# Optimization experiments

Measured on AMD Instinct MI355X. Metric: run time of the kernel, lower is better.

The kernel has to match this reference:

```python
import jax, jax.numpy as jnp
import numpy as np

B, S, H, NH = 2, 2048, 1024, 16
HD = H // NH
R = 4
LORA_SCALE = 16.0 / 4.0  # lora_alpha / r


def lora_linear(x, W, b, A, Bm):
    # x: [b,t,in]; W: [out,in]; A: [r,in]; Bm: [out,r]
    base = jnp.einsum('bti,oi->bto', x, W) + b
    lora = jnp.einsum('btr,or->bto', jnp.einsum('bti,ri->btr', x, A), Bm)
    return base + LORA_SCALE * lora


def setup_inputs() -> dict:
    key = jax.random.key(0)
    ks = jax.random.split(key, 14)
    std = 1.0 / np.sqrt(H)
    d = {
        'hidden_states': jax.random.normal(ks[0], (B, S, H), dtype=jnp.float32),
        'attention_mask': jnp.zeros((B, 1, 1, S), dtype=jnp.float32),
    }
    for i, nm in enumerate(['q', 'k', 'v']):
        d[f'W{nm}'] = jax.random.normal(ks[1 + 4 * i], (H, H), dtype=jnp.float32) * std
        d[f'b{nm}'] = jnp.zeros((H,), dtype=jnp.float32)
        d[f'A{nm}'] = jax.random.normal(ks[2 + 4 * i], (R, H), dtype=jnp.float32) * std
        d[f'B{nm}'] = jnp.zeros((H, R), dtype=jnp.float32) + 0.01 * jax.random.normal(ks[3 + 4 * i], (H, R), dtype=jnp.float32)
    return d


def reference(hidden_states, attention_mask, Wq, bq, Aq, Bq, Wk, bk, Ak, Bk, Wv, bv, Av, Bv):
    def heads(p):  # [b,t,(h d)] -> [b,h,t,d]
        return p.reshape(B, S, NH, HD).transpose(0, 2, 1, 3)

    q = heads(lora_linear(hidden_states, Wq, bq, Aq, Bq))
    k = heads(lora_linear(hidden_states, Wk, bk, Ak, Bk))
    v = heads(lora_linear(hidden_states, Wv, bv, Av, Bv))

    scores = jnp.einsum('bhqd,bhkd->bhqk', q, k) / jnp.sqrt(jnp.float32(HD))
    causal = jnp.tril(jnp.ones((S, S), dtype=scores.dtype))
    causal = (1.0 - causal) * -10000.0  # [S,S], broadcast over b,h
    scores = scores + attention_mask + causal[None, None]
    weights = jax.nn.softmax(scores, axis=-1)  # dropout p=0 -> identity (eval)
    ctx = jnp.einsum('bhqk,bhkd->bhqd', weights, v)
    return ctx.transpose(0, 2, 1, 3).reshape(B, S, H)
```

## Files before the change

### kernel.cpp

```cpp
#include <hip/hip_runtime.h>
#include <stdint.h>

#define B_ 2
#define S_ 2048
#define H_ 1024
#define NH_ 16
#define HD_ 64
#define M_ 4096
#define LOG2E 1.44269504089f

typedef unsigned short u16;
typedef __bf16 bf16x8 __attribute__((ext_vector_type(8)));
typedef float  f32x4  __attribute__((ext_vector_type(4)));

#if __has_builtin(__builtin_amdgcn_exp2f)
#define EXP2(x) __builtin_amdgcn_exp2f(x)
#else
#define EXP2(x) exp2f(x)
#endif

#define WAITV4() asm volatile("s_waitcnt vmcnt(4)" ::: "memory")
#define WAITV0() asm volatile("s_waitcnt vmcnt(0)" ::: "memory")
#define SCHED0() __builtin_amdgcn_sched_barrier(0)

__device__ inline u16 f2bf(float f) {
  union { float f; uint32_t u; } a; a.f = f;
  uint32_t r = a.u + 0x7FFFu + ((a.u >> 16) & 1u);
  return (u16)(r >> 16);
}

__device__ inline void gload_lds16(const void* g, void* l) {
  __builtin_amdgcn_global_load_lds((const __attribute__((address_space(1))) void*)g,
                                   (__attribute__((address_space(3))) void*)l, 16, 0, 0);
}

__global__ __launch_bounds__(256) void cvt_kernel(
    const float* __restrict__ x,
    const float* __restrict__ wq, const float* __restrict__ wk, const float* __restrict__ wv,
    const float* __restrict__ Aq, const float* __restrict__ Ak, const float* __restrict__ Av,
    const float* __restrict__ LBq, const float* __restrict__ LBk, const float* __restrict__ LBv,
    const float* __restrict__ amask,
    u16* __restrict__ xbf, u16* __restrict__ wbf, float* __restrict__ maskl2e) {
  const int XN = M_ * H_;
  const int WN = H_ * H_;
  const int total = XN + 3 * WN;
  int idx = (blockIdx.x * 256 + threadIdx.x) * 4;
  if (idx < XN) {
    float4 v = *(const float4*)(x + idx);
    *(ushort4*)(xbf + idx) = make_ushort4(f2bf(v.x), f2bf(v.y), f2bf(v.z), f2bf(v.w));
  } else if (idx < total) {
    int j = idx - XN; int p = j >> 20; int off = j & (WN - 1);
    const float* W  = (p == 0) ? wq : (p == 1 ? wk : wv);
    const float* A  = (p == 0) ? Aq : (p == 1 ? Ak : Av);
    const float* LB = (p == 0) ? LBq : (p == 1 ? LBk : LBv);
    int n = off >> 10, k = off & 1023;
    float4 v  = *(const float4*)(W + off);
    f32x4 lb  = *(const f32x4*)&LB[n * 4];
    float4 a0 = *(const float4*)(A + k);
    float4 a1 = *(const float4*)(A + 1024 + k);
    float4 a2 = *(const float4*)(A + 2048 + k);
    float4 a3 = *(const float4*)(A + 3072 + k);
    v.x += 4.f * (lb.x * a0.x + lb.y * a1.x + lb.z * a2.x + lb.w * a3.x);
    v.y += 4.f * (lb.x * a0.y + lb.y * a1.y + lb.z * a2.y + lb.w * a3.y);
    v.z += 4.f * (lb.x * a0.z + lb.y * a1.z + lb.z * a2.z + lb.w * a3.z);
    v.w += 4.f * (lb.x * a0.w + lb.y * a1.w + lb.z * a2.w + lb.w * a3.w);
    *(ushort4*)(wbf + (p << 20) + off) = make_ushort4(f2bf(v.x), f2bf(v.y), f2bf(v.z), f2bf(v.w));
  } else {
    int mi = idx - total;
    if (mi < B_ * S_) {
      float4 mv = *(const float4*)(amask + mi);
      mv.x *= LOG2E; mv.y *= LOG2E; mv.z *= LOG2E; mv.w *= LOG2E;
      *(float4*)(maskl2e + mi) = mv;
    }
  }
}

template<int P>
__device__ __forceinline__ void gemm_body(
    const u16* __restrict__ xbf, const u16* __restrict__ wbf,
    const float* __restrict__ bias, u16* __restrict__ qkv,
    u16* __restrict__ As, u16* __restrict__ Bs) {
  const int n0 = blockIdx.x * 128;
  const int m0 = blockIdx.y * 128;
  const u16* Wp = wbf + (P << 20);
  const int tid = threadIdx.x, lane = tid & 63, w = tid >> 6;
  const int g = lane >> 4, q15 = lane & 15;
  const int wr = w >> 1, wc = w & 1;
  const f32x4 fzero = {0.f, 0.f, 0.f, 0.f};
  f32x4 acc[4][4];
#pragma unroll
  for (int mi = 0; mi < 4; ++mi)
#pragma unroll
    for (int ni = 0; ni < 4; ++ni) acc[mi][ni] = fzero;
  const int srow = lane >> 2;

  auto STAGE = [&](int buf, int k0) {
#pragma unroll
    for (int j = 0; j < 2; ++j) {
      int c = w * 2 + j;
      int row = c * 16 + srow;
      int uu = (lane & 3) ^ ((row >> 1) & 3);
      gload_lds16(xbf + (size_t)(m0 + row) * 1024 + k0 + uu * 8, As + buf * 4096 + c * 512);
      gload_lds16(Wp  + (size_t)(n0 + row) * 1024 + k0 + uu * 8, Bs + buf * 4096 + c * 512);
    }
  };

  STAGE(0, 0);
  STAGE(1, 32);
  int c0 = 0, c1 = 1, c2 = 2;
#pragma unroll 1
  for (int t = 0; t < 32; ++t) {
    if (t < 31) WAITV4(); else WAITV0();
    SCHED0();
    __builtin_amdgcn_s_barrier();
    if (t + 2 < 32) STAGE(c2, (t + 2) * 32);
    const u16* Ab = As + c0 * 4096;
    const u16* Bb = Bs + c0 * 4096;
    bf16x8 af[4], bfr[4];
#pragma unroll
    for (int mi = 0; mi < 4; ++mi) {
      int r = wr * 64 + mi * 16 + q15;
      af[mi] = *(const bf16x8*)&Ab[r * 32 + ((g ^ ((r >> 1) & 3)) * 8)];
    }
#pragma unroll
    for (int ni = 0; ni < 4; ++ni) {
      int r = wc * 64 + ni * 16 + q15;
      bfr[ni] = *(const bf16x8*)&Bb[r * 32 + ((g ^ ((r >> 1) & 3)) * 8)];
    }
    __builtin_amdgcn_s_setprio(1);
#pragma unroll
    for (int mi = 0; mi < 4; ++mi)
#pragma unroll
      for (int ni = 0; ni < 4; ++ni) {
        if (P == 2)
          acc[mi][ni] = __builtin_amdgcn_mfma_f32_16x16x32_bf16(af[mi], bfr[ni], acc[mi][ni], 0, 0, 0);
        else
          acc[mi][ni] = __builtin_amdgcn_mfma_f32_16x16x32_bf16(bfr[ni], af[mi], acc[mi][ni], 0, 0, 0);
      }
    __builtin_amdgcn_s_setprio(0);
    int tmp = c0; c0 = c1; c1 = c2; c2 = tmp;
  }

  if (P != 2) {
#pragma unroll
    for (int ni = 0; ni < 4; ++ni) {
      int nb = n0 + wc * 64 + ni * 16 + g * 4;
      f32x4 bi = *(const f32x4*)&bias[nb];
      int h = nb >> 6, dbase = nb & 63;
#pragma unroll
      for (int mi = 0; mi < 4; ++mi) {
        int m = m0 + wr * 64 + mi * 16 + q15;
        int bb = m >> 11, s = m & 2047;
        size_t bhs = (size_t)(bb * 16 + h) * 2048 + s;
        float v0 = acc[mi][ni][0] + bi.x, v1 = acc[mi][ni][1] + bi.y;
        float v2 = acc[mi][ni][2] + bi.z, v3 = acc[mi][ni][3] + bi.w;
        size_t addr;
        if (P == 0) {
          const float qs = 0.125f * LOG2E;
          v0 *= qs; v1 *= qs; v2 *= qs; v3 *= qs;
          addr = bhs * 64 + dbase;
        } else {
          int pos = (((dbase >> 3) ^ (s & 7)) << 3) | (dbase & 7);
          addr = 4194304 + bhs * 64 + pos;
        }
        *(ushort4*)&qkv[addr] = make_ushort4(f2bf(v0), f2bf(v1), f2bf(v2), f2bf(v3));
      }
    }
  } else {
    float biasv[4];
#pragma unroll
    for (int ni = 0; ni < 4; ++ni) biasv[ni] = bias[n0 + wc * 64 + ni * 16 + q15];
#pragma unroll
    for (int mi = 0; mi < 4; ++mi) {
      int mbase = m0 + wr * 64 + mi * 16 + g * 4;
      int bb = mbase >> 11, sbase = mbase & 2047;
      int sr = sbase & 31;
      int cba = (((sr >> 4) & 1) << 2) | (((sr >> 2) & 3) << 3);
      int sp = (sbase & 32) | cba;
#pragma unroll
      for (int ni = 0; ni < 4; ++ni) {
        int n = n0 + wc * 64 + ni * 16 + q15;
        int d = n & 63, h = n >> 6;
        int spp = (((sp >> 3) ^ (d & 7)) << 3) | (sp & 7);
        size_t addr = 8388608 + ((size_t)(bb * 16 + h) * 64 + d) * 2048 + (sbase & ~63) + spp;
        *(ushort4*)&qkv[addr] = make_ushort4(
            f2bf(acc[mi][ni][0] + biasv[ni]), f2bf(acc[mi][ni][1] + biasv[ni]),
            f2bf(acc[mi][ni][2] + biasv[ni]), f2bf(acc[mi][ni][3] + biasv[ni]));
      }
    }
  }
}

__global__ __launch_bounds__(256) void qkv_gemm(
    const u16* __restrict__ xbf, const u16* __restrict__ wbf,
    const float* __restrict__ bq, const float* __restrict__ bk, const float* __restrict__ bv,
    u16* __restrict__ qkv) {
  __shared__ __align__(16) u16 As[3 * 4096];
  __shared__ __align__(16) u16 Bs[3 * 4096];
  switch (blockIdx.z) {
    case 0: gemm_body<0>(xbf, wbf, bq, qkv, As, Bs); break;
    case 1: gemm_body<1>(xbf, wbf, bk, qkv, As, Bs); break;
    default: gemm_body<2>(xbf, wbf, bv, qkv, As, Bs); break;
  }
}

__global__ __launch_bounds__(256, 4) void attn_kernel(
    const u16* __restrict__ qkv, const float* __restrict__ maskl2e, float* __restrict__ out) {
  const int bid = blockIdx.x;
  const int bh = (bid & 7) * 4 + ((bid >> 3) & 3);
  const int qt = 31 - (bid >> 5);
  const int b = bh >> 4, h = bh & 15;
  const int tid = threadIdx.x, lane = tid & 63, w = tid >> 6;
  const int g = lane >> 4, ql = lane & 15;
  const u16* Qb = qkv + (size_t)bh * 131072;
  const u16* Kb = qkv + 4194304 + (size_t)bh * 131072;
  const u16* Vb = qkv + 8388608 + (size_t)bh * 131072;
  const float* Mb = maskl2e + b * 2048;
  __shared__ __align__(16) u16 Ks[2][64][64];
  __shared__ __align__(16) u16 Vs[2][64][64];
  const f32x4 fzero = {0.f, 0.f, 0.f, 0.f};

  auto STAGE = [&](int nb, int kb) {
#pragma unroll
    for (int j = 0; j < 2; ++j) {
      int rl = w * 16 + j * 8 + (lane >> 3);
      gload_lds16(Kb + (size_t)(kb + rl) * 64 + (lane & 7) * 8, &Ks[nb][w * 16 + j * 8][0]);
      gload_lds16(Vb + (size_t)rl * 2048 + kb + (lane & 7) * 8, &Vs[nb][w * 16 + j * 8][0]);
    }
  };

  const int qw = qt * 64 + w * 16;
  const int q  = qw + ql;
  bf16x8 qf[2];
#pragma unroll
  for (int ks = 0; ks < 2; ++ks)
    qf[ks] = *(const bf16x8*)&Qb[(size_t)q * 64 + ks * 32 + g * 8];
  f32x4 acc[4];
#pragma unroll
  for (int dt = 0; dt < 4; ++dt) acc[dt] = fzero;
  float mrun = -1e30f, lrun = 0.f;
  const int nt = qt + 1;

  f32x4 mkC[4], mkN[4];
  STAGE(0, 0);
#pragma unroll
  for (int k16 = 0; k16 < 4; ++k16) mkC[k16] = *(const f32x4*)&Mb[k16 * 16 + g * 4];

#pragma unroll 1
  for (int t = 0; t < nt; ++t) {
    WAITV0();
    SCHED0();
    __builtin_amdgcn_s_barrier();
    const int kb = t * 64;
    if (t + 1 < nt) {
      STAGE((t + 1) & 1, kb + 64);
#pragma unroll
      for (int k16 = 0; k16 < 4; ++k16) mkN[k16] = *(const f32x4*)&Mb[kb + 64 + k16 * 16 + g * 4];
    }
    const int cb = t & 1;
    f32x4 st[4];
    __builtin_amdgcn_s_setprio(1);
#pragma unroll
    for (int k16 = 0; k16 < 4; ++k16) {
      bf16x8 kf0 = *(const bf16x8*)&Ks[cb][k16 * 16 + ql][(g ^ (ql & 7)) * 8];
      bf16x8 kf1 = *(const bf16x8*)&Ks[cb][k16 * 16 + ql][((4 + g) ^ (ql & 7)) * 8];
      st[k16] = __builtin_amdgcn_mfma_f32_16x16x32_bf16(kf0, qf[0], mkC[k16], 0, 0, 0);
      st[k16] = __builtin_amdgcn_mfma_f32_16x16x32_bf16(kf1, qf[1], st[k16], 0, 0, 0);
    }
    __builtin_amdgcn_s_setprio(0);
    const bool needm = (t == nt - 1);
    float sc[16];
#pragma unroll
    for (int k16 = 0; k16 < 4; ++k16)
#pragma unroll
      for (int r = 0; r < 4; ++r) {
        float sv = st[k16][r];
        if (needm) { int key = kb + k16 * 16 + g * 4 + r; sv = (key > q) ? -1e30f : sv; }
        sc[k16 * 4 + r] = sv;
      }
    float t0 = fmaxf(fmaxf(sc[0],  sc[1]),  sc[2]);
    float t1 = fmaxf(fmaxf(sc[3],  sc[4]),  sc[5]);
    float t2 = fmaxf(fmaxf(sc[6],  sc[7]),  sc[8]);
    float t3 = fmaxf(fmaxf(sc[9],  sc[10]), sc[11]);
    float t4 = fmaxf(fmaxf(sc[12], sc[13]), sc[14]);
    float u0 = fmaxf(fmaxf(t0, t1), t2);
    float u1 = fmaxf(fmaxf(t3, t4), sc[15]);
    float pmax = fmaxf(u0, u1);
    if (!__all(pmax <= mrun + 8.f)) {
      float pm = fmaxf(pmax, __shfl_xor(pmax, 16, 64));
      pm = fmaxf(pm, __shfl_xor(pm, 32, 64));
      const float mt = fmaxf(mrun, pm);
      const float scale = EXP2(mrun - mt);
      lrun *= scale;
#pragma unroll
      for (int dt = 0; dt < 4; ++dt) acc[dt] *= scale;
      mrun = mt;
    }
    float pv[16];
#pragma unroll
    for (int i = 0; i < 16; ++i) pv[i] = EXP2(sc[i] - mrun);
    float s8[8], s4[4];
#pragma unroll
    for (int i = 0; i < 8; ++i) s8[i] = pv[i] + pv[i + 8];
#pragma unroll
    for (int i = 0; i < 4; ++i) s4[i] = s8[i] + s8[i + 4];
    lrun += (s4[0] + s4[1]) + (s4[2] + s4[3]);
    bf16x8 pfv[2];
#pragma unroll
    for (int ksub = 0; ksub < 2; ++ksub)
#pragma unroll
      for (int j = 0; j < 4; ++j) {
        pfv[ksub][j]     = (__bf16)pv[ksub * 8 + j];
        pfv[ksub][4 + j] = (__bf16)pv[ksub * 8 + 4 + j];
      }
    __builtin_amdgcn_s_setprio(1);
#pragma unroll
    for (int dt = 0; dt < 4; ++dt)
#pragma unroll
      for (int ksub = 0; ksub < 2; ++ksub) {
        bf16x8 vf = *(const bf16x8*)&Vs[cb][dt * 16 + ql][((ksub * 4 + g) ^ (ql & 7)) * 8];
        acc[dt] = __builtin_amdgcn_mfma_f32_16x16x32_bf16(vf, pfv[ksub], acc[dt], 0, 0, 0);
      }
    __builtin_amdgcn_s_setprio(0);
#pragma unroll
    for (int k16 = 0; k16 < 4; ++k16) mkC[k16] = mkN[k16];
  }

  float lsum = lrun;
  lsum += __shfl_xor(lsum, 16, 64);
  lsum += __shfl_xor(lsum, 32, 64);
  const float inv = 1.f / lsum;
#pragma unroll
  for (int dt = 0; dt < 4; ++dt) {
    f32x4 o = acc[dt] * inv;
    *(f32x4*)&out[((size_t)b * 2048 + q) * 1024 + h * 64 + dt * 16 + g * 4] = o;
  }
}

extern "C" void kernel_launch(void* const* d_in, const int* in_sizes, int n_in,
                              void* d_out, int out_size, void* d_ws, size_t ws_size,
                              hipStream_t stream) {
  const float* x  = (const float*)d_in[0];
  const float* am = (const float*)d_in[1];
  const float* Wq = (const float*)d_in[2];
  const float* bq = (const float*)d_in[3];
  const float* Aq = (const float*)d_in[4];
  const float* Bq = (const float*)d_in[5];
  const float* Wk = (const float*)d_in[6];
  const float* bk = (const float*)d_in[7];
  const float* Ak = (const float*)d_in[8];
  const float* Bk = (const float*)d_in[9];
  const float* Wv = (const float*)d_in[10];
  const float* bv = (const float*)d_in[11];
  const float* Av = (const float*)d_in[12];
  const float* Bv = (const float*)d_in[13];
  float* out = (float*)d_out;

  u16* xbf   = (u16*)d_ws;
  u16* wbf   = xbf + 4194304;
  u16* qkv   = wbf + 3145728;
  float* mk  = (float*)(qkv + 12582912);

  cvt_kernel<<<7172, 256, 0, stream>>>(x, Wq, Wk, Wv, Aq, Ak, Av, Bq, Bk, Bv, am, xbf, wbf, mk);
  qkv_gemm<<<dim3(8, 32, 3), 256, 0, stream>>>(xbf, wbf, bq, bk, bv, qkv);
  attn_kernel<<<1024, 256, 0, stream>>>(qkv, mk, out);
}
```

Before: 92.64 us.

## Load K fragments directly to registers and stage mask in LDS

Drops the LDS staging buffer for K and has each lane load its swizzled K fragments straight from global memory into registers, prefetching the next tile after the QK MFMAs. The additive mask is copied into LDS once per block and added to the scores after the MFMA, replacing per-tile global mask loads that were used as the MFMA accumulator init. This removes LDS traffic and shared memory for K, but adds register pressure (8 bf16x8 per lane) and uncoalesced global K reads that each wave issues redundantly. The global-load wait at the top of the loop now also waits on the K register prefetch.

```diff
diff --git a/kernel.cpp b/kernel.cpp
--- a/kernel.cpp
+++ b/kernel.cpp
@@ -211,20 +211,25 @@
   const int qt = 31 - (bid >> 5);
   const int b = bh >> 4, h = bh & 15;
   const int tid = threadIdx.x, lane = tid & 63, w = tid >> 6;
-  const int g = lane >> 4, ql = lane & 15;
+  const int g = lane >> 4, ql = lane & 15, m7 = ql & 7;
   const u16* Qb = qkv + (size_t)bh * 131072;
   const u16* Kb = qkv + 4194304 + (size_t)bh * 131072;
   const u16* Vb = qkv + 8388608 + (size_t)bh * 131072;
-  const float* Mb = maskl2e + b * 2048;
-  __shared__ __align__(16) u16 Ks[2][64][64];
   __shared__ __align__(16) u16 Vs[2][64][64];
+  __shared__ __align__(16) float MaskL[2048];
   const f32x4 fzero = {0.f, 0.f, 0.f, 0.f};
 
-  auto STAGE = [&](int nb, int kb) {
+  {
+    int o = tid * 4;
+#pragma unroll
+    for (int i = 0; i < 2; ++i)
+      *(float4*)&MaskL[o + i * 1024] = *(const float4*)&maskl2e[b * 2048 + o + i * 1024];
+  }
+
+  auto STAGEV = [&](int nb, int kb) {
 #pragma unroll
     for (int j = 0; j < 2; ++j) {
       int rl = w * 16 + j * 8 + (lane >> 3);
-      gload_lds16(Kb + (size_t)(kb + rl) * 64 + (lane & 7) * 8, &Ks[nb][w * 16 + j * 8][0]);
       gload_lds16(Vb + (size_t)rl * 2048 + kb + (lane & 7) * 8, &Vs[nb][w * 16 + j * 8][0]);
     }
   };
@@ -241,10 +246,14 @@
   float mrun = -1e30f, lrun = 0.f;
   const int nt = qt + 1;
 
-  f32x4 mkC[4], mkN[4];
-  STAGE(0, 0);
-#pragma unroll
-  for (int k16 = 0; k16 < 4; ++k16) mkC[k16] = *(const f32x4*)&Mb[k16 * 16 + g * 4];
+  bf16x8 kA[8];
+#define LOADK(KT) do { const int kb_ = (KT) * 64; \
+  _Pragma("unroll") for (int k16 = 0; k16 < 4; ++k16) { \
+    kA[k16*2]   = *(const bf16x8*)&Kb[(size_t)(kb_ + k16*16 + ql) * 64 + ((g ^ m7) * 8)]; \
+    kA[k16*2+1] = *(const bf16x8*)&Kb[(size_t)(kb_ + k16*16 + ql) * 64 + (((4 + g) ^ m7) * 8)]; } } while (0)
+
+  STAGEV(0, 0);
+  LOADK(0);
 
 #pragma unroll 1
   for (int t = 0; t < nt; ++t) {
@@ -252,29 +261,27 @@
     SCHED0();
     __builtin_amdgcn_s_barrier();
     const int kb = t * 64;
-    if (t + 1 < nt) {
-      STAGE((t + 1) & 1, kb + 64);
-#pragma unroll
-      for (int k16 = 0; k16 < 4; ++k16) mkN[k16] = *(const f32x4*)&Mb[kb + 64 + k16 * 16 + g * 4];
-    }
+    if (t + 1 < nt) STAGEV((t + 1) & 1, kb + 64);
     const int cb = t & 1;
     f32x4 st[4];
     __builtin_amdgcn_s_setprio(1);
 #pragma unroll
     for (int k16 = 0; k16 < 4; ++k16) {
-      bf16x8 kf0 = *(const bf16x8*)&Ks[cb][k16 * 16 + ql][(g ^ (ql & 7)) * 8];
-      bf16x8 kf1 = *(const bf16x8*)&Ks[cb][k16 * 16 + ql][((4 + g) ^ (ql & 7)) * 8];
-      st[k16] = __builtin_amdgcn_mfma_f32_16x16x32_bf16(kf0, qf[0], mkC[k16], 0, 0, 0);
-      st[k16] = __builtin_amdgcn_mfma_f32_16x16x32_bf16(kf1, qf[1], st[k16], 0, 0, 0);
+      st[k16] = __builtin_amdgcn_mfma_f32_16x16x32_bf16(kA[k16*2],   qf[0], fzero,   0, 0, 0);
+      st[k16] = __builtin_amdgcn_mfma_f32_16x16x32_bf16(kA[k16*2+1], qf[1], st[k16], 0, 0, 0);
     }
     __builtin_amdgcn_s_setprio(0);
+    if (t + 1 < nt) LOADK(t + 1);
+    f32x4 mk[4];
+#pragma unroll
+    for (int k16 = 0; k16 < 4; ++k16) mk[k16] = *(const f32x4*)&MaskL[kb + k16 * 16 + g * 4];
     const bool needm = (t == nt - 1);
     float sc[16];
 #pragma unroll
     for (int k16 = 0; k16 < 4; ++k16)
 #pragma unroll
       for (int r = 0; r < 4; ++r) {
-        float sv = st[k16][r];
+        float sv = st[k16][r] + mk[k16][r];
         if (needm) { int key = kb + k16 * 16 + g * 4 + r; sv = (key > q) ? -1e30f : sv; }
         sc[k16 * 4 + r] = sv;
       }
@@ -318,12 +325,10 @@
     for (int dt = 0; dt < 4; ++dt)
 #pragma unroll
       for (int ksub = 0; ksub < 2; ++ksub) {
-        bf16x8 vf = *(const bf16x8*)&Vs[cb][dt * 16 + ql][((ksub * 4 + g) ^ (ql & 7)) * 8];
+        bf16x8 vf = *(const bf16x8*)&Vs[cb][dt * 16 + ql][((ksub * 4 + g) ^ m7) * 8];
         acc[dt] = __builtin_amdgcn_mfma_f32_16x16x32_bf16(vf, pfv[ksub], acc[dt], 0, 0, 0);
       }
     __builtin_amdgcn_s_setprio(0);
-#pragma unroll
-    for (int k16 = 0; k16 < 4; ++k16) mkC[k16] = mkN[k16];
   }
 
   float lsum = lrun;
@@ -335,6 +340,7 @@
     f32x4 o = acc[dt] * inv;
     *(f32x4*)&out[((size_t)b * 2048 + q) * 1024 + h * 64 + dt * 16 + g * 4] = o;
   }
+#undef LOADK
 }
 
 extern "C" void kernel_launch(void* const* d_in, const int* in_sizes, int n_in,
```

New measurement: 93.50 us. About the same (+0.9%).

## Pair causal q-tiles per block and run two heads per 512-thread workgroup

Applied to the files above, without the earlier changes.

The attention kernel moves from 1024 blocks of 256 threads to 256 persistent blocks of 512 threads. Each block holds two independent 4-wave pipelines, one per head, and each pipeline processes q-tile a and then q-tile 31-a, so every block does the same total causal work. The mask row is now loaded once into LDS and added after the QK MFMA, replacing the per-tile global mask prefetch into the accumulator. This removes the causal load imbalance and the tail effect, at the cost of one wave per SIMD, a block-wide barrier shared by both pipelines, and less latency hiding.

```diff
diff --git a/kernel.cpp b/kernel.cpp
--- a/kernel.cpp
+++ b/kernel.cpp
@@ -21,6 +21,7 @@
 
 #define WAITV4() asm volatile("s_waitcnt vmcnt(4)" ::: "memory")
 #define WAITV0() asm volatile("s_waitcnt vmcnt(0)" ::: "memory")
+#define LGKM0()  asm volatile("s_waitcnt lgkmcnt(0)" ::: "memory")
 #define SCHED0() __builtin_amdgcn_sched_barrier(0)
 
 __device__ inline u16 f2bf(float f) {
@@ -204,136 +205,140 @@
   }
 }
 
-__global__ __launch_bounds__(256, 4) void attn_kernel(
+__global__ __launch_bounds__(512, 1) void attn_kernel(
     const u16* __restrict__ qkv, const float* __restrict__ maskl2e, float* __restrict__ out) {
   const int bid = blockIdx.x;
-  const int bh = (bid & 7) * 4 + ((bid >> 3) & 3);
-  const int qt = 31 - (bid >> 5);
+  const int xcd = bid & 7, rr = bid >> 3;
+  const int a = rr >> 1, bp = rr & 1;
+  const int tid = threadIdx.x, lane = tid & 63, w = tid >> 6;
+  const int pipe = w >> 2, wp = w & 3;
+  const int bh = xcd * 4 + bp * 2 + pipe;
   const int b = bh >> 4, h = bh & 15;
-  const int tid = threadIdx.x, lane = tid & 63, w = tid >> 6;
   const int g = lane >> 4, ql = lane & 15;
   const u16* Qb = qkv + (size_t)bh * 131072;
   const u16* Kb = qkv + 4194304 + (size_t)bh * 131072;
   const u16* Vb = qkv + 8388608 + (size_t)bh * 131072;
-  const float* Mb = maskl2e + b * 2048;
-  __shared__ __align__(16) u16 Ks[2][64][64];
-  __shared__ __align__(16) u16 Vs[2][64][64];
+  __shared__ __align__(16) u16 Ks[2][2][64][64];
+  __shared__ __align__(16) u16 Vs[2][2][64][64];
+  __shared__ __align__(16) float MaskL[2048];
   const f32x4 fzero = {0.f, 0.f, 0.f, 0.f};
 
+  *(float4*)&MaskL[tid * 4] = *(const float4*)&maskl2e[b * 2048 + tid * 4];
+  LGKM0();
+  SCHED0();
+
   auto STAGE = [&](int nb, int kb) {
 #pragma unroll
     for (int j = 0; j < 2; ++j) {
-      int rl = w * 16 + j * 8 + (lane >> 3);
-      gload_lds16(Kb + (size_t)(kb + rl) * 64 + (lane & 7) * 8, &Ks[nb][w * 16 + j * 8][0]);
-      gload_lds16(Vb + (size_t)rl * 2048 + kb + (lane & 7) * 8, &Vs[nb][w * 16 + j * 8][0]);
+      int rl = wp * 16 + j * 8 + (lane >> 3);
+      gload_lds16(Kb + (size_t)(kb + rl) * 64 + (lane & 7) * 8, &Ks[pipe][nb][rl][0]);
+      gload_lds16(Vb + (size_t)rl * 2048 + kb + (lane & 7) * 8, &Vs[pipe][nb][rl][0]);
     }
   };
 
-  const int qw = qt * 64 + w * 16;
-  const int q  = qw + ql;
-  bf16x8 qf[2];
-#pragma unroll
-  for (int ks = 0; ks < 2; ++ks)
-    qf[ks] = *(const bf16x8*)&Qb[(size_t)q * 64 + ks * 32 + g * 8];
-  f32x4 acc[4];
-#pragma unroll
-  for (int dt = 0; dt < 4; ++dt) acc[dt] = fzero;
-  float mrun = -1e30f, lrun = 0.f;
-  const int nt = qt + 1;
-
-  f32x4 mkC[4], mkN[4];
-  STAGE(0, 0);
-#pragma unroll
-  for (int k16 = 0; k16 < 4; ++k16) mkC[k16] = *(const f32x4*)&Mb[k16 * 16 + g * 4];
-
 #pragma unroll 1
-  for (int t = 0; t < nt; ++t) {
-    WAITV0();
-    SCHED0();
-    __builtin_amdgcn_s_barrier();
-    const int kb = t * 64;
-    if (t + 1 < nt) {
-      STAGE((t + 1) & 1, kb + 64);
-#pragma unroll
-      for (int k16 = 0; k16 < 4; ++k16) mkN[k16] = *(const f32x4*)&Mb[kb + 64 + k16 * 16 + g * 4];
-    }
-    const int cb = t & 1;
-    f32x4 st[4];
-    __builtin_amdgcn_s_setprio(1);
-#pragma unroll
-    for (int k16 = 0; k16 < 4; ++k16) {
-      bf16x8 kf0 = *(const bf16x8*)&Ks[cb][k16 * 16 + ql][(g ^ (ql & 7)) * 8];
-      bf16x8 kf1 = *(const bf16x8*)&Ks[cb][k16 * 16 + ql][((4 + g) ^ (ql & 7)) * 8];
-      st[k16] = __builtin_amdgcn_mfma_f32_16x16x32_bf16(kf0, qf[0], mkC[k16], 0, 0, 0);
-      st[k16] = __builtin_amdgcn_mfma_f32_16x16x32_bf16(kf1, qf[1], st[k16], 0, 0, 0);
-    }
-    __builtin_amdgcn_s_setprio(0);
-    const bool needm = (t == nt - 1);
-    float sc[16];
-#pragma unroll
-    for (int k16 = 0; k16 < 4; ++k16)
-#pragma unroll
-      for (int r = 0; r < 4; ++r) {
-        float sv = st[k16][r];
-        if (needm) { int key = kb + k16 * 16 + g * 4 + r; sv = (key > q) ? -1e30f : sv; }
-        sc[k16 * 4 + r] = sv;
-      }
-    float t0 = fmaxf(fmaxf(sc[0],  sc[1]),  sc[2]);
-    float t1 = fmaxf(fmaxf(sc[3],  sc[4]),  sc[5]);
-    float t2 = fmaxf(fmaxf(sc[6],  sc[7]),  sc[8]);
-    float t3 = fmaxf(fmaxf(sc[9],  sc[10]), sc[11]);
-    float t4 = fmaxf(fmaxf(sc[12], sc[13]), sc[14]);
-    float u0 = fmaxf(fmaxf(t0, t1), t2);
-    float u1 = fmaxf(fmaxf(t3, t4), sc[15]);
-    float pmax = fmaxf(u0, u1);
-    if (!__all(pmax <= mrun + 8.f)) {
-      float pm = fmaxf(pmax, __shfl_xor(pmax, 16, 64));
-      pm = fmaxf(pm, __shfl_xor(pm, 32, 64));
-      const float mt = fmaxf(mrun, pm);
-      const float scale = EXP2(mrun - mt);
-      lrun *= scale;
-#pragma unroll
-      for (int dt = 0; dt < 4; ++dt) acc[dt] *= scale;
-      mrun = mt;
-    }
-    float pv[16];
-#pragma unroll
-    for (int i = 0; i < 16; ++i) pv[i] = EXP2(sc[i] - mrun);
-    float s8[8], s4[4];
-#pragma unroll
-    for (int i = 0; i < 8; ++i) s8[i] = pv[i] + pv[i + 8];
-#pragma unroll
-    for (int i = 0; i < 4; ++i) s4[i] = s8[i] + s8[i + 4];
-    lrun += (s4[0] + s4[1]) + (s4[2] + s4[3]);
-    bf16x8 pfv[2];
-#pragma unroll
-    for (int ksub = 0; ksub < 2; ++ksub)
-#pragma unroll
-      for (int j = 0; j < 4; ++j) {
-        pfv[ksub][j]     = (__bf16)pv[ksub * 8 + j];
-        pfv[ksub][4 + j] = (__bf16)pv[ksub * 8 + 4 + j];
-      }
-    __builtin_amdgcn_s_setprio(1);
-#pragma unroll
-    for (int dt = 0; dt < 4; ++dt)
-#pragma unroll
-      for (int ksub = 0; ksub < 2; ++ksub) {
-        bf16x8 vf = *(const bf16x8*)&Vs[cb][dt * 16 + ql][((ksub * 4 + g) ^ (ql & 7)) * 8];
-        acc[dt] = __builtin_amdgcn_mfma_f32_16x16x32_bf16(vf, pfv[ksub], acc[dt], 0, 0, 0);
-      }
-    __builtin_amdgcn_s_setprio(0);
-#pragma unroll
-    for (int k16 = 0; k16 < 4; ++k16) mkC[k16] = mkN[k16];
-  }
-
-  float lsum = lrun;
-  lsum += __shfl_xor(lsum, 16, 64);
-  lsum += __shfl_xor(lsum, 32, 64);
-  const float inv = 1.f / lsum;
-#pragma unroll
-  for (int dt = 0; dt < 4; ++dt) {
-    f32x4 o = acc[dt] * inv;
-    *(f32x4*)&out[((size_t)b * 2048 + q) * 1024 + h * 64 + dt * 16 + g * 4] = o;
+  for (int ph = 0; ph < 2; ++ph) {
+    const int qt = ph ? (31 - a) : a;
+    const int nt = qt + 1;
+    const int qw = qt * 64 + wp * 16;
+    const int q  = qw + ql;
+    bf16x8 qf[2];
+#pragma unroll
+    for (int ks = 0; ks < 2; ++ks)
+      qf[ks] = *(const bf16x8*)&Qb[(size_t)q * 64 + ks * 32 + g * 8];
+    f32x4 acc[4];
+#pragma unroll
+    for (int dt = 0; dt < 4; ++dt) acc[dt] = fzero;
+    float mrun = -1e30f, lrun = 0.f;
+
+    STAGE(0, 0);
+#pragma unroll 1
+    for (int t = 0; t < nt; ++t) {
+      WAITV0();
+      SCHED0();
+      __builtin_amdgcn_s_barrier();
+      const int kb = t * 64;
+      if (t + 1 < nt) STAGE((t + 1) & 1, kb + 64);
+      const int cb = t & 1;
+      f32x4 st[4];
+      __builtin_amdgcn_s_setprio(1);
+#pragma unroll
+      for (int k16 = 0; k16 < 4; ++k16) {
+        bf16x8 kf0 = *(const bf16x8*)&Ks[pipe][cb][k16 * 16 + ql][(g ^ (ql & 7)) * 8];
+        bf16x8 kf1 = *(const bf16x8*)&Ks[pipe][cb][k16 * 16 + ql][((4 + g) ^ (ql & 7)) * 8];
+        st[k16] = __builtin_amdgcn_mfma_f32_16x16x32_bf16(kf0, qf[0], fzero,   0, 0, 0);
+        st[k16] = __builtin_amdgcn_mfma_f32_16x16x32_bf16(kf1, qf[1], st[k16], 0, 0, 0);
+      }
+      __builtin_amdgcn_s_setprio(0);
+      f32x4 mk[4];
+#pragma unroll
+      for (int k16 = 0; k16 < 4; ++k16) mk[k16] = *(const f32x4*)&MaskL[kb + k16 * 16 + g * 4];
+      const bool needm = (t == nt - 1);
+      float sc[16];
+#pragma unroll
+      for (int k16 = 0; k16 < 4; ++k16)
+#pragma unroll
+        for (int r = 0; r < 4; ++r) {
+          float sv = st[k16][r] + mk[k16][r];
+          if (needm) { int key = kb + k16 * 16 + g * 4 + r; sv = (key > q) ? -1e30f : sv; }
+          sc[k16 * 4 + r] = sv;
+        }
+      float t0 = fmaxf(fmaxf(sc[0],  sc[1]),  sc[2]);
+      float t1 = fmaxf(fmaxf(sc[3],  sc[4]),  sc[5]);
+      float t2 = fmaxf(fmaxf(sc[6],  sc[7]),  sc[8]);
+      float t3 = fmaxf(fmaxf(sc[9],  sc[10]), sc[11]);
+      float t4 = fmaxf(fmaxf(sc[12], sc[13]), sc[14]);
+      float u0 = fmaxf(fmaxf(t0, t1), t2);
+      float u1 = fmaxf(fmaxf(t3, t4), sc[15]);
+      float pmax = fmaxf(u0, u1);
+      if (!__all(pmax <= mrun + 8.f)) {
+        float pm = fmaxf(pmax, __shfl_xor(pmax, 16, 64));
+        pm = fmaxf(pm, __shfl_xor(pm, 32, 64));
+        const float mt = fmaxf(mrun, pm);
+        const float scale = EXP2(mrun - mt);
+        lrun *= scale;
+#pragma unroll
+        for (int dt = 0; dt < 4; ++dt) acc[dt] *= scale;
+        mrun = mt;
+      }
+      float pv[16];
+#pragma unroll
+      for (int i = 0; i < 16; ++i) pv[i] = EXP2(sc[i] - mrun);
+      float s8[8], s4[4];
+#pragma unroll
+      for (int i = 0; i < 8; ++i) s8[i] = pv[i] + pv[i + 8];
+#pragma unroll
+      for (int i = 0; i < 4; ++i) s4[i] = s8[i] + s8[i + 4];
+      lrun += (s4[0] + s4[1]) + (s4[2] + s4[3]);
+      bf16x8 pfv[2];
+#pragma unroll
+      for (int ksub = 0; ksub < 2; ++ksub)
+#pragma unroll
+        for (int j = 0; j < 4; ++j) {
+          pfv[ksub][j]     = (__bf16)pv[ksub * 8 + j];
+          pfv[ksub][4 + j] = (__bf16)pv[ksub * 8 + 4 + j];
+        }
+      __builtin_amdgcn_s_setprio(1);
+#pragma unroll
+      for (int dt = 0; dt < 4; ++dt)
+#pragma unroll
+        for (int ksub = 0; ksub < 2; ++ksub) {
+          bf16x8 vf = *(const bf16x8*)&Vs[pipe][cb][dt * 16 + ql][((ksub * 4 + g) ^ (ql & 7)) * 8];
+          acc[dt] = __builtin_amdgcn_mfma_f32_16x16x32_bf16(vf, pfv[ksub], acc[dt], 0, 0, 0);
+        }
+      __builtin_amdgcn_s_setprio(0);
+    }
+
+    float lsum = lrun;
+    lsum += __shfl_xor(lsum, 16, 64);
+    lsum += __shfl_xor(lsum, 32, 64);
+    const float inv = 1.f / lsum;
+#pragma unroll
+    for (int dt = 0; dt < 4; ++dt) {
+      f32x4 o = acc[dt] * inv;
+      *(f32x4*)&out[((size_t)b * 2048 + q) * 1024 + h * 64 + dt * 16 + g * 4] = o;
+    }
+    __syncthreads();
   }
 }
 
@@ -363,5 +368,5 @@
 
   cvt_kernel<<<7172, 256, 0, stream>>>(x, Wq, Wk, Wv, Aq, Ak, Av, Bq, Bk, Bv, am, xbf, wbf, mk);
   qkv_gemm<<<dim3(8, 32, 3), 256, 0, stream>>>(xbf, wbf, bq, bk, bv, qkv);
-  attn_kernel<<<1024, 256, 0, stream>>>(qkv, mk, out);
-}
+  attn_kernel<<<256, 512, 0, stream>>>(qkv, mk, out);
+}
```

Result: slower. 95.43 us (+3.0%).

## Enlarge QKV GEMM tiles to 256x256 with 512 threads and stage mask in LDS

Applied to the files above, without the earlier changes.

The QKV projection GEMM moves from 128x128 tiles with a 3-stage BK=32 pipeline to 256x256 tiles, 8 waves, BK=64, double buffering, and global loads interleaved between MFMA groups. The aim is more reuse per LDS byte and fewer global loads per flop. The cost is a grid of only 192 blocks on a 256-CU part, plus a full vmcnt(0) wait each iteration. Separately, the attention kernel loads the additive mask into LDS once per block and adds it after QK^T, instead of prefetching it from global into the MFMA accumulator every iteration.

```diff
diff --git a/kernel.cpp b/kernel.cpp
--- a/kernel.cpp
+++ b/kernel.cpp
@@ -19,8 +19,8 @@
 #define EXP2(x) exp2f(x)
 #endif
 
-#define WAITV4() asm volatile("s_waitcnt vmcnt(4)" ::: "memory")
 #define WAITV0() asm volatile("s_waitcnt vmcnt(0)" ::: "memory")
+#define LGKM0()  asm volatile("s_waitcnt lgkmcnt(0)" ::: "memory")
 #define SCHED0() __builtin_amdgcn_sched_barrier(0)
 
 __device__ inline u16 f2bf(float f) {
@@ -80,76 +80,139 @@
     const u16* __restrict__ xbf, const u16* __restrict__ wbf,
     const float* __restrict__ bias, u16* __restrict__ qkv,
     u16* __restrict__ As, u16* __restrict__ Bs) {
-  const int n0 = blockIdx.x * 128;
-  const int m0 = blockIdx.y * 128;
+  const int n0 = blockIdx.x * 256;
+  const int m0 = blockIdx.y * 256;
   const u16* Wp = wbf + (P << 20);
   const int tid = threadIdx.x, lane = tid & 63, w = tid >> 6;
-  const int g = lane >> 4, q15 = lane & 15;
-  const int wr = w >> 1, wc = w & 1;
+  const int g = lane >> 4, q15 = lane & 15, q7 = q15 & 7;
+  const int wm = w >> 2, wn = w & 3;
   const f32x4 fzero = {0.f, 0.f, 0.f, 0.f};
-  f32x4 acc[4][4];
-#pragma unroll
-  for (int mi = 0; mi < 4; ++mi)
+  f32x4 acc[8][4];
+#pragma unroll
+  for (int mi = 0; mi < 8; ++mi)
 #pragma unroll
     for (int ni = 0; ni < 4; ++ni) acc[mi][ni] = fzero;
-  const int srow = lane >> 2;
-
-  auto STAGE = [&](int buf, int k0) {
-#pragma unroll
-    for (int j = 0; j < 2; ++j) {
-      int c = w * 2 + j;
-      int row = c * 16 + srow;
-      int uu = (lane & 3) ^ ((row >> 1) & 3);
-      gload_lds16(xbf + (size_t)(m0 + row) * 1024 + k0 + uu * 8, As + buf * 4096 + c * 512);
-      gload_lds16(Wp  + (size_t)(n0 + row) * 1024 + k0 + uu * 8, Bs + buf * 4096 + c * 512);
+
+  const int srow8 = lane >> 3;
+  const int suu   = (lane & 7) ^ srow8;
+
+  auto STAGE_A2 = [&](int buf, int k0, int half) {
+#pragma unroll
+    for (int i = half * 2; i < half * 2 + 2; ++i) {
+      int rbase = w * 32 + i * 8;
+      gload_lds16(xbf + (size_t)(m0 + rbase + srow8) * 1024 + k0 + suu * 8,
+                  As + buf * 16384 + rbase * 64);
     }
   };
-
-  STAGE(0, 0);
-  STAGE(1, 32);
-  int c0 = 0, c1 = 1, c2 = 2;
+  auto STAGE_B2 = [&](int buf, int k0, int half) {
+#pragma unroll
+    for (int i = half * 2; i < half * 2 + 2; ++i) {
+      int rbase = w * 32 + i * 8;
+      gload_lds16(Wp + (size_t)(n0 + rbase + srow8) * 1024 + k0 + suu * 8,
+                  Bs + buf * 16384 + rbase * 64);
+    }
+  };
+
+  STAGE_A2(0, 0, 0); STAGE_A2(0, 0, 1);
+  STAGE_B2(0, 0, 0); STAGE_B2(0, 0, 1);
+
 #pragma unroll 1
-  for (int t = 0; t < 32; ++t) {
-    if (t < 31) WAITV4(); else WAITV0();
+  for (int t = 0; t < 16; ++t) {
+    WAITV0();
     SCHED0();
     __builtin_amdgcn_s_barrier();
-    if (t + 2 < 32) STAGE(c2, (t + 2) * 32);
-    const u16* Ab = As + c0 * 4096;
-    const u16* Bb = Bs + c0 * 4096;
-    bf16x8 af[4], bfr[4];
-#pragma unroll
-    for (int mi = 0; mi < 4; ++mi) {
-      int r = wr * 64 + mi * 16 + q15;
-      af[mi] = *(const bf16x8*)&Ab[r * 32 + ((g ^ ((r >> 1) & 3)) * 8)];
-    }
+    const int cb = t & 1, nb = (t + 1) & 1;
+    const int k1 = (t + 1) * 64;
+    const bool nx = (t + 1 < 16);
+    const u16* Ab = As + cb * 16384;
+    const u16* Bb = Bs + cb * 16384;
+
+    bf16x8 af[8];
+    if (nx) STAGE_A2(nb, k1, 0);
+#pragma unroll
+    for (int mi = 0; mi < 8; ++mi)
+      af[mi] = *(const bf16x8*)&Ab[(wm * 128 + mi * 16 + q15) * 64 + ((g ^ q7) * 8)];
+    {
+      bf16x8 b0 = *(const bf16x8*)&Bb[(wn * 64 + 0 * 16 + q15) * 64 + ((g ^ q7) * 8)];
+      bf16x8 b1 = *(const bf16x8*)&Bb[(wn * 64 + 1 * 16 + q15) * 64 + ((g ^ q7) * 8)];
+      __builtin_amdgcn_s_setprio(1);
+#pragma unroll
+      for (int mi = 0; mi < 8; ++mi) {
+        if (P == 2) {
+          acc[mi][0] = __builtin_amdgcn_mfma_f32_16x16x32_bf16(af[mi], b0, acc[mi][0], 0, 0, 0);
+          acc[mi][1] = __builtin_amdgcn_mfma_f32_16x16x32_bf16(af[mi], b1, acc[mi][1], 0, 0, 0);
+        } else {
+          acc[mi][0] = __builtin_amdgcn_mfma_f32_16x16x32_bf16(b0, af[mi], acc[mi][0], 0, 0, 0);
+          acc[mi][1] = __builtin_amdgcn_mfma_f32_16x16x32_bf16(b1, af[mi], acc[mi][1], 0, 0, 0);
+        }
+      }
+      __builtin_amdgcn_s_setprio(0);
+    }
+    if (nx) STAGE_A2(nb, k1, 1);
+    {
+      bf16x8 b2 = *(const bf16x8*)&Bb[(wn * 64 + 2 * 16 + q15) * 64 + ((g ^ q7) * 8)];
+      bf16x8 b3 = *(const bf16x8*)&Bb[(wn * 64 + 3 * 16 + q15) * 64 + ((g ^ q7) * 8)];
+      __builtin_amdgcn_s_setprio(1);
+#pragma unroll
+      for (int mi = 0; mi < 8; ++mi) {
+        if (P == 2) {
+          acc[mi][2] = __builtin_amdgcn_mfma_f32_16x16x32_bf16(af[mi], b2, acc[mi][2], 0, 0, 0);
+          acc[mi][3] = __builtin_amdgcn_mfma_f32_16x16x32_bf16(af[mi], b3, acc[mi][3], 0, 0, 0);
+        } else {
+          acc[mi][2] = __builtin_amdgcn_mfma_f32_16x16x32_bf16(b2, af[mi], acc[mi][2], 0, 0, 0);
+          acc[mi][3] = __builtin_amdgcn_mfma_f32_16x16x32_bf16(b3, af[mi], acc[mi][3], 0, 0, 0);
+        }
+      }
+      __builtin_amdgcn_s_setprio(0);
+    }
+    if (nx) STAGE_B2(nb, k1, 0);
+#pragma unroll
+    for (int mi = 0; mi < 8; ++mi)
+      af[mi] = *(const bf16x8*)&Ab[(wm * 128 + mi * 16 + q15) * 64 + (((4 + g) ^ q7) * 8)];
+    {
+      bf16x8 b0 = *(const bf16x8*)&Bb[(wn * 64 + 0 * 16 + q15) * 64 + (((4 + g) ^ q7) * 8)];
+      bf16x8 b1 = *(const bf16x8*)&Bb[(wn * 64 + 1 * 16 + q15) * 64 + (((4 + g) ^ q7) * 8)];
+      __builtin_amdgcn_s_setprio(1);
+#pragma unroll
+      for (int mi = 0; mi < 8; ++mi) {
+        if (P == 2) {
+          acc[mi][0] = __builtin_amdgcn_mfma_f32_16x16x32_bf16(af[mi], b0, acc[mi][0], 0, 0, 0);
+          acc[mi][1] = __builtin_amdgcn_mfma_f32_16x16x32_bf16(af[mi], b1, acc[mi][1], 0, 0, 0);
+        } else {
+          acc[mi][0] = __builtin_amdgcn_mfma_f32_16x16x32_bf16(b0, af[mi], acc[mi][0], 0, 0, 0);
+          acc[mi][1] = __builtin_amdgcn_mfma_f32_16x16x32_bf16(b1, af[mi], acc[mi][1], 0, 0, 0);
+        }
+      }
+      __builtin_amdgcn_s_setprio(0);
+    }
+    if (nx) STAGE_B2(nb, k1, 1);
+    {
+      bf16x8 b2 = *(const bf16x8*)&Bb[(wn * 64 + 2 * 16 + q15) * 64 + (((4 + g) ^ q7) * 8)];
+      bf16x8 b3 = *(const bf16x8*)&Bb[(wn * 64 + 3 * 16 + q15) * 64 + (((4 + g) ^ q7) * 8)];
+      __builtin_amdgcn_s_setprio(1);
+#pragma unroll
+      for (int mi = 0; mi < 8; ++mi) {
+        if (P == 2) {
+          acc[mi][2] = __builtin_amdgcn_mfma_f32_16x16x32_bf16(af[mi], b2, acc[mi][2], 0, 0, 0);
+          acc[mi][3] = __builtin_amdgcn_mfma_f32_16x16x32_bf16(af[mi], b3, acc[mi][3], 0, 0, 0);
+        } else {
+          acc[mi][2] = __builtin_amdgcn_mfma_f32_16x16x32_bf16(b2, af[mi], acc[mi][2], 0, 0, 0);
+          acc[mi][3] = __builtin_amdgcn_mfma_f32_16x16x32_bf16(b3, af[mi], acc[mi][3], 0, 0, 0);
+        }
+      }
+      __builtin_amdgcn_s_setprio(0);
+    }
+  }
+
+  if (P != 2) {
 #pragma unroll
     for (int ni = 0; ni < 4; ++ni) {
-      int r = wc * 64 + ni * 16 + q15;
-      bfr[ni] = *(const bf16x8*)&Bb[r * 32 + ((g ^ ((r >> 1) & 3)) * 8)];
-    }
-    __builtin_amdgcn_s_setprio(1);
-#pragma unroll
-    for (int mi = 0; mi < 4; ++mi)
-#pragma unroll
-      for (int ni = 0; ni < 4; ++ni) {
-        if (P == 2)
-          acc[mi][ni] = __builtin_amdgcn_mfma_f32_16x16x32_bf16(af[mi], bfr[ni], acc[mi][ni], 0, 0, 0);
-        else
-          acc[mi][ni] = __builtin_amdgcn_mfma_f32_16x16x32_bf16(bfr[ni], af[mi], acc[mi][ni], 0, 0, 0);
-      }
-    __builtin_amdgcn_s_setprio(0);
-    int tmp = c0; c0 = c1; c1 = c2; c2 = tmp;
-  }
-
-  if (P != 2) {
-#pragma unroll
-    for (int ni = 0; ni < 4; ++ni) {
-      int nb = n0 + wc * 64 + ni * 16 + g * 4;
+      int nb = n0 + wn * 64 + ni * 16 + g * 4;
       f32x4 bi = *(const f32x4*)&bias[nb];
       int h = nb >> 6, dbase = nb & 63;
 #pragma unroll
-      for (int mi = 0; mi < 4; ++mi) {
-        int m = m0 + wr * 64 + mi * 16 + q15;
+      for (int mi = 0; mi < 8; ++mi) {
+        int m = m0 + wm * 128 + mi * 16 + q15;
         int bb = m >> 11, s = m & 2047;
         size_t bhs = (size_t)(bb * 16 + h) * 2048 + s;
         float v0 = acc[mi][ni][0] + bi.x, v1 = acc[mi][ni][1] + bi.y;
@@ -169,17 +232,17 @@
   } else {
     float biasv[4];
 #pragma unroll
-    for (int ni = 0; ni < 4; ++ni) biasv[ni] = bias[n0 + wc * 64 + ni * 16 + q15];
-#pragma unroll
-    for (int mi = 0; mi < 4; ++mi) {
-      int mbase = m0 + wr * 64 + mi * 16 + g * 4;
+    for (int ni = 0; ni < 4; ++ni) biasv[ni] = bias[n0 + wn * 64 + ni * 16 + q15];
+#pragma unroll
+    for (int mi = 0; mi < 8; ++mi) {
+      int mbase = m0 + wm * 128 + mi * 16 + g * 4;
       int bb = mbase >> 11, sbase = mbase & 2047;
       int sr = sbase & 31;
       int cba = (((sr >> 4) & 1) << 2) | (((sr >> 2) & 3) << 3);
       int sp = (sbase & 32) | cba;
 #pragma unroll
       for (int ni = 0; ni < 4; ++ni) {
-        int n = n0 + wc * 64 + ni * 16 + q15;
+        int n = n0 + wn * 64 + ni * 16 + q15;
         int d = n & 63, h = n >> 6;
         int spp = (((sp >> 3) ^ (d & 7)) << 3) | (sp & 7);
         size_t addr = 8388608 + ((size_t)(bb * 16 + h) * 64 + d) * 2048 + (sbase & ~63) + spp;
@@ -191,12 +254,12 @@
   }
 }
 
-__global__ __launch_bounds__(256) void qkv_gemm(
+__global__ __launch_bounds__(512, 2) void qkv_gemm(
     const u16* __restrict__ xbf, const u16* __restrict__ wbf,
     const float* __restrict__ bq, const float* __restrict__ bk, const float* __restrict__ bv,
     u16* __restrict__ qkv) {
-  __shared__ __align__(16) u16 As[3 * 4096];
-  __shared__ __align__(16) u16 Bs[3 * 4096];
+  __shared__ __align__(16) u16 As[2 * 16384];
+  __shared__ __align__(16) u16 Bs[2 * 16384];
   switch (blockIdx.z) {
     case 0: gemm_body<0>(xbf, wbf, bq, qkv, As, Bs); break;
     case 1: gemm_body<1>(xbf, wbf, bk, qkv, As, Bs); break;
@@ -215,10 +278,18 @@
   const u16* Qb = qkv + (size_t)bh * 131072;
   const u16* Kb = qkv + 4194304 + (size_t)bh * 131072;
   const u16* Vb = qkv + 8388608 + (size_t)bh * 131072;
-  const float* Mb = maskl2e + b * 2048;
   __shared__ __align__(16) u16 Ks[2][64][64];
   __shared__ __align__(16) u16 Vs[2][64][64];
+  __shared__ __align__(16) float MaskL[2048];
   const f32x4 fzero = {0.f, 0.f, 0.f, 0.f};
+
+  {
+    int o = tid * 4;
+    *(float4*)&MaskL[o]        = *(const float4*)&maskl2e[b * 2048 + o];
+    *(float4*)&MaskL[o + 1024] = *(const float4*)&maskl2e[b * 2048 + o + 1024];
+  }
+  LGKM0();
+  SCHED0();
 
   auto STAGE = [&](int nb, int kb) {
 #pragma unroll
@@ -241,22 +312,14 @@
   float mrun = -1e30f, lrun = 0.f;
   const int nt = qt + 1;
 
-  f32x4 mkC[4], mkN[4];
   STAGE(0, 0);
-#pragma unroll
-  for (int k16 = 0; k16 < 4; ++k16) mkC[k16] = *(const f32x4*)&Mb[k16 * 16 + g * 4];
-
 #pragma unroll 1
   for (int t = 0; t < nt; ++t) {
     WAITV0();
     SCHED0();
     __builtin_amdgcn_s_barrier();
     const int kb = t * 64;
-    if (t + 1 < nt) {
-      STAGE((t + 1) & 1, kb + 64);
-#pragma unroll
-      for (int k16 = 0; k16 < 4; ++k16) mkN[k16] = *(const f32x4*)&Mb[kb + 64 + k16 * 16 + g * 4];
-    }
+    if (t + 1 < nt) STAGE((t + 1) & 1, kb + 64);
     const int cb = t & 1;
     f32x4 st[4];
     __builtin_amdgcn_s_setprio(1);
@@ -264,17 +327,20 @@
     for (int k16 = 0; k16 < 4; ++k16) {
       bf16x8 kf0 = *(const bf16x8*)&Ks[cb][k16 * 16 + ql][(g ^ (ql & 7)) * 8];
       bf16x8 kf1 = *(const bf16x8*)&Ks[cb][k16 * 16 + ql][((4 + g) ^ (ql & 7)) * 8];
-      st[k16] = __builtin_amdgcn_mfma_f32_16x16x32_bf16(kf0, qf[0], mkC[k16], 0, 0, 0);
+      st[k16] = __builtin_amdgcn_mfma_f32_16x16x32_bf16(kf0, qf[0], fzero,   0, 0, 0);
       st[k16] = __builtin_amdgcn_mfma_f32_16x16x32_bf16(kf1, qf[1], st[k16], 0, 0, 0);
     }
     __builtin_amdgcn_s_setprio(0);
+    f32x4 mk[4];
+#pragma unroll
+    for (int k16 = 0; k16 < 4; ++k16) mk[k16] = *(const f32x4*)&MaskL[kb + k16 * 16 + g * 4];
     const bool needm = (t == nt - 1);
     float sc[16];
 #pragma unroll
     for (int k16 = 0; k16 < 4; ++k16)
 #pragma unroll
       for (int r = 0; r < 4; ++r) {
-        float sv = st[k16][r];
+        float sv = st[k16][r] + mk[k16][r];
         if (needm) { int key = kb + k16 * 16 + g * 4 + r; sv = (key > q) ? -1e30f : sv; }
         sc[k16 * 4 + r] = sv;
       }
@@ -322,8 +388,6 @@
         acc[dt] = __builtin_amdgcn_mfma_f32_16x16x32_bf16(vf, pfv[ksub], acc[dt], 0, 0, 0);
       }
     __builtin_amdgcn_s_setprio(0);
-#pragma unroll
-    for (int k16 = 0; k16 < 4; ++k16) mkC[k16] = mkN[k16];
   }
 
   float lsum = lrun;
@@ -362,6 +426,6 @@
   float* mk  = (float*)(qkv + 12582912);
 
   cvt_kernel<<<7172, 256, 0, stream>>>(x, Wq, Wk, Wv, Aq, Ak, Av, Bq, Bk, Bv, am, xbf, wbf, mk);
-  qkv_gemm<<<dim3(8, 32, 3), 256, 0, stream>>>(xbf, wbf, bq, bk, bv, qkv);
+  qkv_gemm<<<dim3(4, 16, 3), 512, 0, stream>>>(xbf, wbf, bq, bk, bv, qkv);
   attn_kernel<<<1024, 256, 0, stream>>>(qkv, mk, out);
 }
```

Result: slower. 95.22 us (+2.8%).
